# Optimization experiments

Hardware: AMD Instinct MI355X
Metric: run time of the kernel (lower is better)

## Reference

```python
import jax, jax.numpy as jnp
import numpy as np

S = 8192        # seq_length
H2 = 1024       # 2 * lstm_hidden_size
A = 2048        # attention_hidden_size
E = 768         # embedding_dim == pos_embedding_dim


def _bahdanau_weights(sentence, length, ctx, W_s, b_s, W_c, b_c, v, b_v):
    # sentence: [1, S, H2], ctx: [1, E_ctx]
    u = jnp.einsum('bsh,ha->bsa', sentence, W_s) + b_s \
        + (ctx @ W_c + b_c)[:, None, :]                    # [1, S, A]
    e = jnp.einsum('bsa,a->bs', jnp.tanh(u), v) + b_v       # [1, S]
    mask = jnp.arange(S)[None, :] >= length[:, None]        # [1, S] key mask
    e = jnp.where(mask, -jnp.inf, e)
    all_inf = jnp.all(mask, axis=1)                         # [1]
    # guard fully-masked rows so softmax stays finite, then zero them (matches torch)
    e_safe = jnp.where(all_inf[:, None], jnp.zeros_like(e), e)
    w = jax.nn.softmax(e_safe, axis=1)
    return jnp.where(all_inf[:, None], 0.0, w)              # [1, S]


def setup_inputs() -> dict:
    key = jax.random.key(0)
    ks = jax.random.split(key, 24)
    f = jax.random.normal
    sc_s = 1.0 / np.sqrt(H2)
    sc_c = 1.0 / np.sqrt(E)
    sc_v = 1.0 / np.sqrt(A)
    inp = {
        'sentence': f(ks[0], (1, S, H2), jnp.float32),
        'length': jax.random.randint(ks[1], (1,), 0, S),
        'pos_embedding': f(ks[2], (1, E), jnp.float32),
        'cardinal_phrase_embedding': f(ks[3], (1, E), jnp.float32),
        'headline_embedding': f(ks[4], (1, E), jnp.float32),
    }
    i = 5
    for tag in ('p', 'c', 'h'):
        inp[f'W_sent_{tag}'] = f(ks[i], (H2, A), jnp.float32) * sc_s; i += 1
        inp[f'b_sent_{tag}'] = f(ks[i], (A,), jnp.float32) * sc_s; i += 1
        inp[f'W_ctx_{tag}'] = f(ks[i], (E, A), jnp.float32) * sc_c; i += 1
        inp[f'b_ctx_{tag}'] = f(ks[i], (A,), jnp.float32) * sc_c; i += 1
        inp[f'v_{tag}'] = f(ks[i], (A,), jnp.float32) * sc_v; i += 1
        inp[f'bv_{tag}'] = f(ks[i], (), jnp.float32) * sc_v; i += 1
    return inp


def reference(sentence, length, pos_embedding, cardinal_phrase_embedding,
              headline_embedding,
              W_sent_p, b_sent_p, W_ctx_p, b_ctx_p, v_p, bv_p,
              W_sent_c, b_sent_c, W_ctx_c, b_ctx_c, v_c, bv_c,
              W_sent_h, b_sent_h, W_ctx_h, b_ctx_h, v_h, bv_h):
    w_pos = _bahdanau_weights(sentence, length, pos_embedding,
                              W_sent_p, b_sent_p, W_ctx_p, b_ctx_p, v_p, bv_p)
    w_card = _bahdanau_weights(sentence, length, cardinal_phrase_embedding,
                               W_sent_c, b_sent_c, W_ctx_c, b_ctx_c, v_c, bv_c)
    w_head = _bahdanau_weights(sentence, length, headline_embedding,
                               W_sent_h, b_sent_h, W_ctx_h, b_ctx_h, v_h, bv_h)
    fused = (w_pos + w_card + w_head) / 3.0                 # [1, S]
    return jnp.einsum('bs,bsh->bh', fused, sentence)        # [1, H2]
```

## Files before the change

kernel.cpp:

```cpp
#include <hip/hip_runtime.h>
#include <hip/hip_bf16.h>
#include <stdint.h>


namespace {

constexpr int S = 8192;
constexpr int H = 1024;
constexpr int A = 2048;
constexpr int E = 768;

typedef __bf16 bf16x8 __attribute__((ext_vector_type(8)));
typedef float f32x4 __attribute__((ext_vector_type(4)));

__device__ __forceinline__ void gl_lds16(const void* g, void* l) {
  __builtin_amdgcn_global_load_lds(
      (const __attribute__((address_space(1))) void*)g,
      (__attribute__((address_space(3))) void*)l, 16, 0, 0);
}

__global__ __launch_bounds__(256)
void k_prep(const float* __restrict__ sentence, __bf16* __restrict__ sentB,
            const float* __restrict__ Wp, const float* __restrict__ Wc_s,
            const float* __restrict__ Wh, __bf16* __restrict__ WtB,
            const float* __restrict__ ctx_p, const float* __restrict__ ctx_c,
            const float* __restrict__ ctx_h,
            const float* __restrict__ Wcx_p, const float* __restrict__ Wcx_c,
            const float* __restrict__ Wcx_h,
            const float* __restrict__ bs_p, const float* __restrict__ bs_c,
            const float* __restrict__ bs_h,
            const float* __restrict__ bc_p, const float* __restrict__ bc_c,
            const float* __restrict__ bc_h,
            float* __restrict__ ctxb, float* __restrict__ e_arr,
            float* __restrict__ outz, const int* __restrict__ length) {
  __shared__ float tile[64][65];
  __shared__ float part[4][64];
  int b = blockIdx.x;
  int t = threadIdx.x;

  if (b < 4096) {
    int len = min(max(length[0], 0), S);
    if (b * 2 >= len) return;
    int g = b * 256 + t;
    const float4* s4 = (const float4*)sentence + (size_t)g * 2;
    float4 a = s4[0], c = s4[1];
    bf16x8 o;
    o[0] = (__bf16)a.x; o[1] = (__bf16)a.y; o[2] = (__bf16)a.z; o[3] = (__bf16)a.w;
    o[4] = (__bf16)c.x; o[5] = (__bf16)c.y; o[6] = (__bf16)c.z; o[7] = (__bf16)c.w;
    *((bf16x8*)sentB + g) = o;
  } else if (b < 5632) {
    int r = b - 4096;
    int head = r >> 9; r &= 511;
    const float* W = head == 0 ? Wp : (head == 1 ? Wc_s : Wh);
    __bf16* dst = WtB + (size_t)head * A * H;
    int a0 = (r & 31) * 64;
    int k0 = (r >> 5) * 64;
#pragma unroll
    for (int i = 0; i < 16; ++i) {
      int idx = t + i * 256;
      int rr = idx >> 6, cc = idx & 63;
      tile[cc][rr] = W[(size_t)(k0 + rr) * A + a0 + cc];
    }
    __syncthreads();
    int al = t >> 3, kg = (t & 7) * 8;
#pragma unroll
    for (int half = 0; half < 2; ++half) {
      int aa = al + half * 32;
      bf16x8 o;
#pragma unroll
      for (int j = 0; j < 8; ++j) o[j] = (__bf16)tile[aa][kg + j];
      *(bf16x8*)&dst[(size_t)(a0 + aa) * H + k0 + kg] = o;
    }
  } else if (b < 5728) {
    int r = b - 5632;
    int head = r >> 5; r &= 31;
    const float* ctx = head == 0 ? ctx_p : (head == 1 ? ctx_c : ctx_h);
    const float* Wc  = head == 0 ? Wcx_p : (head == 1 ? Wcx_c : Wcx_h);
    int a0 = r * 64;
    int al = t & 63, slice = t >> 6;
    int a = a0 + al;
    float s = 0.f;
    int e0 = slice * 192;
#pragma unroll 8
    for (int e = e0; e < e0 + 192; ++e) s = fmaf(ctx[e], Wc[(size_t)e * A + a], s);
    part[slice][al] = s;
    __syncthreads();
    if (t < 64) {
      const float* bs = head == 0 ? bs_p : (head == 1 ? bs_c : bs_h);
      const float* bc = head == 0 ? bc_p : (head == 1 ? bc_c : bc_h);
      ctxb[head * A + a0 + t] = part[0][t] + part[1][t] + part[2][t] + part[3][t]
                              + bs[a0 + t] + bc[a0 + t];
    }
  } else if (b < 5752) {
    int g = (b - 5728) * 256 + t;
    ((float4*)e_arr)[g] = (float4){0.f, 0.f, 0.f, 0.f};
  } else {
    ((float4*)outz)[t] = (float4){0.f, 0.f, 0.f, 0.f};
  }
}

__global__ __launch_bounds__(256)
void k_gemm_e(const __bf16* __restrict__ sentB, const __bf16* __restrict__ WtB,
              const float* __restrict__ ctxb,
              const float* __restrict__ v_p, const float* __restrict__ v_c,
              const float* __restrict__ v_h,
              const int* __restrict__ length, float* __restrict__ e_out) {
  int m0 = blockIdx.x * 128;
  int len = length[0];
  if (m0 >= len) return;
  int n0 = blockIdx.y * 128;
  int head = blockIdx.z;
  const float* v  = head == 0 ? v_p : (head == 1 ? v_c : v_h);
  const __bf16* Wt = WtB + (size_t)head * A * H;
  const float* cb = ctxb + head * A;
  float* e_h = e_out + head * S;

  __shared__ __align__(16) __bf16 lsA[128 * 32];
  __shared__ __align__(16) __bf16 lsB[128 * 32];
  __shared__ float e_part[128];

  int tid = threadIdx.x;
  if (tid < 128) e_part[tid] = 0.f;

  int lane = tid & 63;
  int wave = tid >> 6;
  int wm = wave >> 1, wn = wave & 1;
  int quad = lane >> 4, l16 = lane & 15;

  f32x4 acc[4][4];
#pragma unroll
  for (int i = 0; i < 4; ++i)
#pragma unroll
    for (int j = 0; j < 4; ++j) acc[i][j] = (f32x4){0.f, 0.f, 0.f, 0.f};

  const __bf16* gA0 = sentB + (size_t)(m0 + (tid >> 2)) * H + ((tid & 3) * 8);
  const __bf16* gA1 = gA0 + (size_t)64 * H;
  const __bf16* gB0 = Wt + (size_t)(n0 + (tid >> 2)) * H + ((tid & 3) * 8);
  const __bf16* gB1 = gB0 + (size_t)64 * H;

  for (int k0 = 0; k0 < H; k0 += 32) {
    __syncthreads();
    gl_lds16(gA0 + k0, lsA + tid * 8);
    gl_lds16(gA1 + k0, lsA + 2048 + tid * 8);
    gl_lds16(gB0 + k0, lsB + tid * 8);
    gl_lds16(gB1 + k0, lsB + 2048 + tid * 8);
    __syncthreads();

    bf16x8 af[4], bfv[4];
#pragma unroll
    for (int i = 0; i < 4; ++i) {
      af[i]  = *(const bf16x8*)&lsA[(wm * 64 + i * 16 + l16) * 32 + quad * 8];
      bfv[i] = *(const bf16x8*)&lsB[(wn * 64 + i * 16 + l16) * 32 + quad * 8];
    }
#pragma unroll
    for (int i = 0; i < 4; ++i)
#pragma unroll
      for (int j = 0; j < 4; ++j)
        acc[i][j] = __builtin_amdgcn_mfma_f32_16x16x32_bf16(af[i], bfv[j], acc[i][j], 0, 0, 0);
  }

  float vj[4], cbj[4];
#pragma unroll
  for (int j = 0; j < 4; ++j) {
    int col = n0 + wn * 64 + j * 16 + l16;
    vj[j] = v[col];
    cbj[j] = cb[col];
  }
#pragma unroll
  for (int i = 0; i < 4; ++i) {
#pragma unroll
    for (int r = 0; r < 4; ++r) {
      float p = 0.f;
#pragma unroll
      for (int j = 0; j < 4; ++j) {
        float u = acc[i][j][r] + cbj[j];
        float ex = __expf(2.f * u);
        float th = 1.f - 2.f / (ex + 1.f);
        p = fmaf(th, vj[j], p);
      }
      p += __shfl_xor(p, 1);
      p += __shfl_xor(p, 2);
      p += __shfl_xor(p, 4);
      p += __shfl_xor(p, 8);
      if (l16 == 0) atomicAdd(&e_part[wm * 64 + i * 16 + quad * 4 + r], p);
    }
  }
  __syncthreads();
  if (tid < 128) atomicAdd(&e_h[m0 + tid], e_part[tid]);
}

__global__ __launch_bounds__(1024)
void k_sum(const float* __restrict__ e_arr, const int* __restrict__ length,
           float* __restrict__ sums) {
  int head = blockIdx.x;
  const float* e_h = e_arr + head * S;
  int len = min(max(length[0], 0), S);
  int t = threadIdx.x;
  __shared__ float red[16];

  float ss = 0.f;
  int base = t * 8;
#pragma unroll
  for (int j = 0; j < 8; ++j) {
    int s = base + j;
    if (s < len) ss += __expf(e_h[s]);
  }
#pragma unroll
  for (int o = 32; o >= 1; o >>= 1) ss += __shfl_xor(ss, o);
  if ((t & 63) == 0) red[t >> 6] = ss;
  __syncthreads();
  if (t == 0) {
    float tot = 0.f;
#pragma unroll
    for (int i = 0; i < 16; ++i) tot += red[i];
    sums[head] = tot;
  }
}

__global__ void k_out(const float* __restrict__ sent, const float* __restrict__ e_arr,
                      const float* __restrict__ sums, const int* __restrict__ length,
                      float* __restrict__ out) {
  int len = min(max(length[0], 0), S);
  int r0 = blockIdx.x * 32;
  if (r0 >= len) return;
  int col = threadIdx.x * 4;
  int rend = min(r0 + 32, len);
  float i0 = 1.f / sums[0], i1 = 1.f / sums[1], i2 = 1.f / sums[2];
  float4 acc = {0.f, 0.f, 0.f, 0.f};
  for (int r = r0; r < rend; ++r) {
    float w = (__expf(e_arr[r]) * i0 +
               __expf(e_arr[S + r]) * i1 +
               __expf(e_arr[2 * S + r]) * i2) * (1.f / 3.f);
    float4 x = *(const float4*)(sent + (size_t)r * H + col);
    acc.x = fmaf(w, x.x, acc.x);
    acc.y = fmaf(w, x.y, acc.y);
    acc.z = fmaf(w, x.z, acc.z);
    acc.w = fmaf(w, x.w, acc.w);
  }
  atomicAdd(&out[col + 0], acc.x);
  atomicAdd(&out[col + 1], acc.y);
  atomicAdd(&out[col + 2], acc.z);
  atomicAdd(&out[col + 3], acc.w);
}

}

extern "C" void kernel_launch(void* const* d_in, const int* in_sizes, int n_in,
                              void* d_out, int out_size, void* d_ws, size_t ws_size,
                              hipStream_t stream) {
  const float* sentence = (const float*)d_in[0];
  const int* length     = (const int*)d_in[1];
  const float* ctx_p = (const float*)d_in[2];
  const float* ctx_c = (const float*)d_in[3];
  const float* ctx_h = (const float*)d_in[4];
  const float* W_s[3] = {(const float*)d_in[5],  (const float*)d_in[11], (const float*)d_in[17]};
  const float* b_s[3] = {(const float*)d_in[6],  (const float*)d_in[12], (const float*)d_in[18]};
  const float* W_c[3] = {(const float*)d_in[7],  (const float*)d_in[13], (const float*)d_in[19]};
  const float* b_c[3] = {(const float*)d_in[8],  (const float*)d_in[14], (const float*)d_in[20]};
  const float* v_[3]  = {(const float*)d_in[9],  (const float*)d_in[15], (const float*)d_in[21]};
  float* out = (float*)d_out;

  char* ws = (char*)d_ws;
  __bf16* sentB = (__bf16*)(ws);
  __bf16* WtB   = (__bf16*)(ws + 16777216);
  float* ctxb   = (float*)(ws + 29360128);
  float* e_arr  = (float*)(ws + 29384704);
  float* sums   = (float*)(ws + 29483008);

  k_prep<<<5753, 256, 0, stream>>>(sentence, sentB,
                                   W_s[0], W_s[1], W_s[2], WtB,
                                   ctx_p, ctx_c, ctx_h,
                                   W_c[0], W_c[1], W_c[2],
                                   b_s[0], b_s[1], b_s[2],
                                   b_c[0], b_c[1], b_c[2],
                                   ctxb, e_arr, out, length);
  k_gemm_e<<<dim3(S / 128, A / 128, 3), 256, 0, stream>>>(sentB, WtB, ctxb,
                                                          v_[0], v_[1], v_[2], length, e_arr);
  k_sum<<<3, 1024, 0, stream>>>(e_arr, length, sums);
  k_out<<<S / 32, 256, 0, stream>>>(sentence, e_arr, sums, length, out);
}
```

Measured before the change: 234.6 us.

## Fuse all stages into one persistent cooperative kernel with grid syncs

Replaces the four separate launches (prep, GEMM+tanh reduction, softmax sum, weighted output) with a single cooperative kernel of 512 persistent blocks that loop over the former block indices and separate phases with grid.sync. The softmax denominators are now computed redundantly in every block instead of in a separate kernel, removing the sums buffer. This aims to remove inter-kernel launch gaps, at the cost of lower parallelism per phase, grid-wide barrier overhead, and repeated reads of the score array by every block.

```diff
diff --git a/kernel.cpp b/kernel.cpp
--- a/kernel.cpp
+++ b/kernel.cpp
@@ -1,7 +1,10 @@
 #include <hip/hip_runtime.h>
 #include <hip/hip_bf16.h>
+#include <hip/hip_cooperative_groups.h>
 #include <stdint.h>
 
+
+namespace cg = cooperative_groups;
 
 namespace {
 
@@ -9,9 +12,26 @@
 constexpr int H = 1024;
 constexpr int A = 2048;
 constexpr int E = 768;
+constexpr int GRID = 512;
 
 typedef __bf16 bf16x8 __attribute__((ext_vector_type(8)));
 typedef float f32x4 __attribute__((ext_vector_type(4)));
+
+struct KArgs {
+  const float* sentence;
+  const int* length;
+  const float* ctx[3];
+  const float* Ws[3];
+  const float* bs[3];
+  const float* Wc[3];
+  const float* bc[3];
+  const float* v[3];
+  __bf16* sentB;
+  __bf16* WtB;
+  float* ctxb;
+  float* e_arr;
+  float* out;
+};
 
 __device__ __forceinline__ void gl_lds16(const void* g, void* l) {
   __builtin_amdgcn_global_load_lds(
@@ -19,228 +39,206 @@
       (__attribute__((address_space(3))) void*)l, 16, 0, 0);
 }
 
-__global__ __launch_bounds__(256)
-void k_prep(const float* __restrict__ sentence, __bf16* __restrict__ sentB,
-            const float* __restrict__ Wp, const float* __restrict__ Wc_s,
-            const float* __restrict__ Wh, __bf16* __restrict__ WtB,
-            const float* __restrict__ ctx_p, const float* __restrict__ ctx_c,
-            const float* __restrict__ ctx_h,
-            const float* __restrict__ Wcx_p, const float* __restrict__ Wcx_c,
-            const float* __restrict__ Wcx_h,
-            const float* __restrict__ bs_p, const float* __restrict__ bs_c,
-            const float* __restrict__ bs_h,
-            const float* __restrict__ bc_p, const float* __restrict__ bc_c,
-            const float* __restrict__ bc_h,
-            float* __restrict__ ctxb, float* __restrict__ e_arr,
-            float* __restrict__ outz, const int* __restrict__ length) {
-  __shared__ float tile[64][65];
-  __shared__ float part[4][64];
-  int b = blockIdx.x;
-  int t = threadIdx.x;
-
-  if (b < 4096) {
-    int len = min(max(length[0], 0), S);
-    if (b * 2 >= len) return;
-    int g = b * 256 + t;
-    const float4* s4 = (const float4*)sentence + (size_t)g * 2;
-    float4 a = s4[0], c = s4[1];
-    bf16x8 o;
-    o[0] = (__bf16)a.x; o[1] = (__bf16)a.y; o[2] = (__bf16)a.z; o[3] = (__bf16)a.w;
-    o[4] = (__bf16)c.x; o[5] = (__bf16)c.y; o[6] = (__bf16)c.z; o[7] = (__bf16)c.w;
-    *((bf16x8*)sentB + g) = o;
-  } else if (b < 5632) {
-    int r = b - 4096;
-    int head = r >> 9; r &= 511;
-    const float* W = head == 0 ? Wp : (head == 1 ? Wc_s : Wh);
-    __bf16* dst = WtB + (size_t)head * A * H;
-    int a0 = (r & 31) * 64;
-    int k0 = (r >> 5) * 64;
-#pragma unroll
-    for (int i = 0; i < 16; ++i) {
-      int idx = t + i * 256;
-      int rr = idx >> 6, cc = idx & 63;
-      tile[cc][rr] = W[(size_t)(k0 + rr) * A + a0 + cc];
+__global__ __launch_bounds__(256, 2)
+void k_mega(KArgs a) {
+  __shared__ __align__(16) union {
+    struct { float tile[64][65]; float part[4][64]; } p;
+    struct { __bf16 lsA[4096]; __bf16 lsB[4096]; float e_part[128]; } g;
+    struct { float red[3][4]; } o;
+  } sh;
+
+  cg::grid_group grid = cg::this_grid();
+  const int bid = blockIdx.x;
+  const int t = threadIdx.x;
+  const int len = min(max(a.length[0], 0), S);
+
+  for (int it = bid; it < 5753; it += GRID) {
+    if (it < 4096) {
+      if (it * 2 >= len) continue;
+      int g = it * 256 + t;
+      const float4* s4 = (const float4*)a.sentence + (size_t)g * 2;
+      float4 x = s4[0], y = s4[1];
+      bf16x8 o;
+      o[0] = (__bf16)x.x; o[1] = (__bf16)x.y; o[2] = (__bf16)x.z; o[3] = (__bf16)x.w;
+      o[4] = (__bf16)y.x; o[5] = (__bf16)y.y; o[6] = (__bf16)y.z; o[7] = (__bf16)y.w;
+      *((bf16x8*)a.sentB + g) = o;
+    } else if (it < 5632) {
+      int r = it - 4096;
+      int head = r >> 9; r &= 511;
+      const float* W = a.Ws[head];
+      __bf16* dst = a.WtB + (size_t)head * A * H;
+      int a0 = (r & 31) * 64;
+      int k0 = (r >> 5) * 64;
+      __syncthreads();
+#pragma unroll
+      for (int i = 0; i < 16; ++i) {
+        int idx = t + i * 256;
+        int rr = idx >> 6, cc = idx & 63;
+        sh.p.tile[cc][rr] = W[(size_t)(k0 + rr) * A + a0 + cc];
+      }
+      __syncthreads();
+      int al = t >> 3, kg = (t & 7) * 8;
+#pragma unroll
+      for (int half = 0; half < 2; ++half) {
+        int aa = al + half * 32;
+        bf16x8 o;
+#pragma unroll
+        for (int j = 0; j < 8; ++j) o[j] = (__bf16)sh.p.tile[aa][kg + j];
+        *(bf16x8*)&dst[(size_t)(a0 + aa) * H + k0 + kg] = o;
+      }
+    } else if (it < 5728) {
+      int r = it - 5632;
+      int head = r >> 5; r &= 31;
+      const float* cx = a.ctx[head];
+      const float* Wc = a.Wc[head];
+      int a0 = r * 64;
+      int al = t & 63, slice = t >> 6;
+      float s = 0.f;
+      int e0 = slice * 192;
+#pragma unroll 8
+      for (int e = e0; e < e0 + 192; ++e) s = fmaf(cx[e], Wc[(size_t)e * A + a0 + al], s);
+      __syncthreads();
+      sh.p.part[slice][al] = s;
+      __syncthreads();
+      if (t < 64) {
+        a.ctxb[head * A + a0 + t] = sh.p.part[0][t] + sh.p.part[1][t] + sh.p.part[2][t] +
+                                    sh.p.part[3][t] + a.bs[head][a0 + t] + a.bc[head][a0 + t];
+      }
+    } else if (it < 5752) {
+      int g = (it - 5728) * 256 + t;
+      ((float4*)a.e_arr)[g] = (float4){0.f, 0.f, 0.f, 0.f};
+    } else {
+      ((float4*)a.out)[t] = (float4){0.f, 0.f, 0.f, 0.f};
+    }
+  }
+
+  grid.sync();
+
+  for (int j = bid; j < 3072; j += GRID) {
+    int head = j >> 10;
+    int r = j & 1023;
+    int m0 = (r & 63) << 7;
+    int n0 = (r >> 6) << 7;
+    if (m0 >= len) continue;
+
+    const float* v = a.v[head];
+    const __bf16* Wt = a.WtB + (size_t)head * A * H;
+    const float* cb = a.ctxb + head * A;
+    float* e_h = a.e_arr + head * S;
+
+    int lane = t & 63;
+    int wave = t >> 6;
+    int wm = wave >> 1, wn = wave & 1;
+    int quad = lane >> 4, l16 = lane & 15;
+
+    if (t < 128) sh.g.e_part[t] = 0.f;
+
+    f32x4 acc[4][4];
+#pragma unroll
+    for (int i = 0; i < 4; ++i)
+#pragma unroll
+      for (int jj = 0; jj < 4; ++jj) acc[i][jj] = (f32x4){0.f, 0.f, 0.f, 0.f};
+
+    const __bf16* gA0 = a.sentB + (size_t)(m0 + (t >> 2)) * H + ((t & 3) * 8);
+    const __bf16* gA1 = gA0 + (size_t)64 * H;
+    const __bf16* gB0 = Wt + (size_t)(n0 + (t >> 2)) * H + ((t & 3) * 8);
+    const __bf16* gB1 = gB0 + (size_t)64 * H;
+
+    for (int k0 = 0; k0 < H; k0 += 32) {
+      __syncthreads();
+      gl_lds16(gA0 + k0, sh.g.lsA + t * 8);
+      gl_lds16(gA1 + k0, sh.g.lsA + 2048 + t * 8);
+      gl_lds16(gB0 + k0, sh.g.lsB + t * 8);
+      gl_lds16(gB1 + k0, sh.g.lsB + 2048 + t * 8);
+      __syncthreads();
+
+      bf16x8 af[4], bfv[4];
+#pragma unroll
+      for (int i = 0; i < 4; ++i) {
+        af[i]  = *(const bf16x8*)&sh.g.lsA[(wm * 64 + i * 16 + l16) * 32 + quad * 8];
+        bfv[i] = *(const bf16x8*)&sh.g.lsB[(wn * 64 + i * 16 + l16) * 32 + quad * 8];
+      }
+#pragma unroll
+      for (int i = 0; i < 4; ++i)
+#pragma unroll
+        for (int jj = 0; jj < 4; ++jj)
+          acc[i][jj] = __builtin_amdgcn_mfma_f32_16x16x32_bf16(af[i], bfv[jj], acc[i][jj], 0, 0, 0);
+    }
+
+    float vj[4], cbj[4];
+#pragma unroll
+    for (int jj = 0; jj < 4; ++jj) {
+      int col = n0 + wn * 64 + jj * 16 + l16;
+      vj[jj] = v[col];
+      cbj[jj] = cb[col];
+    }
+#pragma unroll
+    for (int i = 0; i < 4; ++i) {
+#pragma unroll
+      for (int rr = 0; rr < 4; ++rr) {
+        float p = 0.f;
+#pragma unroll
+        for (int jj = 0; jj < 4; ++jj) {
+          float u = acc[i][jj][rr] + cbj[jj];
+          float ex = __expf(2.f * u);
+          float th = 1.f - 2.f / (ex + 1.f);
+          p = fmaf(th, vj[jj], p);
+        }
+        p += __shfl_xor(p, 1);
+        p += __shfl_xor(p, 2);
+        p += __shfl_xor(p, 4);
+        p += __shfl_xor(p, 8);
+        if (l16 == 0) atomicAdd(&sh.g.e_part[wm * 64 + i * 16 + quad * 4 + rr], p);
+      }
     }
     __syncthreads();
-    int al = t >> 3, kg = (t & 7) * 8;
-#pragma unroll
-    for (int half = 0; half < 2; ++half) {
-      int aa = al + half * 32;
-      bf16x8 o;
-#pragma unroll
-      for (int j = 0; j < 8; ++j) o[j] = (__bf16)tile[aa][kg + j];
-      *(bf16x8*)&dst[(size_t)(a0 + aa) * H + k0 + kg] = o;
-    }
-  } else if (b < 5728) {
-    int r = b - 5632;
-    int head = r >> 5; r &= 31;
-    const float* ctx = head == 0 ? ctx_p : (head == 1 ? ctx_c : ctx_h);
-    const float* Wc  = head == 0 ? Wcx_p : (head == 1 ? Wcx_c : Wcx_h);
-    int a0 = r * 64;
-    int al = t & 63, slice = t >> 6;
-    int a = a0 + al;
-    float s = 0.f;
-    int e0 = slice * 192;
-#pragma unroll 8
-    for (int e = e0; e < e0 + 192; ++e) s = fmaf(ctx[e], Wc[(size_t)e * A + a], s);
-    part[slice][al] = s;
-    __syncthreads();
-    if (t < 64) {
-      const float* bs = head == 0 ? bs_p : (head == 1 ? bs_c : bs_h);
-      const float* bc = head == 0 ? bc_p : (head == 1 ? bc_c : bc_h);
-      ctxb[head * A + a0 + t] = part[0][t] + part[1][t] + part[2][t] + part[3][t]
-                              + bs[a0 + t] + bc[a0 + t];
-    }
-  } else if (b < 5752) {
-    int g = (b - 5728) * 256 + t;
-    ((float4*)e_arr)[g] = (float4){0.f, 0.f, 0.f, 0.f};
-  } else {
-    ((float4*)outz)[t] = (float4){0.f, 0.f, 0.f, 0.f};
-  }
-}
-
-__global__ __launch_bounds__(256)
-void k_gemm_e(const __bf16* __restrict__ sentB, const __bf16* __restrict__ WtB,
-              const float* __restrict__ ctxb,
-              const float* __restrict__ v_p, const float* __restrict__ v_c,
-              const float* __restrict__ v_h,
-              const int* __restrict__ length, float* __restrict__ e_out) {
-  int m0 = blockIdx.x * 128;
-  int len = length[0];
-  if (m0 >= len) return;
-  int n0 = blockIdx.y * 128;
-  int head = blockIdx.z;
-  const float* v  = head == 0 ? v_p : (head == 1 ? v_c : v_h);
-  const __bf16* Wt = WtB + (size_t)head * A * H;
-  const float* cb = ctxb + head * A;
-  float* e_h = e_out + head * S;
-
-  __shared__ __align__(16) __bf16 lsA[128 * 32];
-  __shared__ __align__(16) __bf16 lsB[128 * 32];
-  __shared__ float e_part[128];
-
-  int tid = threadIdx.x;
-  if (tid < 128) e_part[tid] = 0.f;
-
-  int lane = tid & 63;
-  int wave = tid >> 6;
-  int wm = wave >> 1, wn = wave & 1;
-  int quad = lane >> 4, l16 = lane & 15;
-
-  f32x4 acc[4][4];
-#pragma unroll
-  for (int i = 0; i < 4; ++i)
-#pragma unroll
-    for (int j = 0; j < 4; ++j) acc[i][j] = (f32x4){0.f, 0.f, 0.f, 0.f};
-
-  const __bf16* gA0 = sentB + (size_t)(m0 + (tid >> 2)) * H + ((tid & 3) * 8);
-  const __bf16* gA1 = gA0 + (size_t)64 * H;
-  const __bf16* gB0 = Wt + (size_t)(n0 + (tid >> 2)) * H + ((tid & 3) * 8);
-  const __bf16* gB1 = gB0 + (size_t)64 * H;
-
-  for (int k0 = 0; k0 < H; k0 += 32) {
-    __syncthreads();
-    gl_lds16(gA0 + k0, lsA + tid * 8);
-    gl_lds16(gA1 + k0, lsA + 2048 + tid * 8);
-    gl_lds16(gB0 + k0, lsB + tid * 8);
-    gl_lds16(gB1 + k0, lsB + 2048 + tid * 8);
-    __syncthreads();
-
-    bf16x8 af[4], bfv[4];
-#pragma unroll
-    for (int i = 0; i < 4; ++i) {
-      af[i]  = *(const bf16x8*)&lsA[(wm * 64 + i * 16 + l16) * 32 + quad * 8];
-      bfv[i] = *(const bf16x8*)&lsB[(wn * 64 + i * 16 + l16) * 32 + quad * 8];
-    }
-#pragma unroll
-    for (int i = 0; i < 4; ++i)
-#pragma unroll
-      for (int j = 0; j < 4; ++j)
-        acc[i][j] = __builtin_amdgcn_mfma_f32_16x16x32_bf16(af[i], bfv[j], acc[i][j], 0, 0, 0);
-  }
-
-  float vj[4], cbj[4];
-#pragma unroll
-  for (int j = 0; j < 4; ++j) {
-    int col = n0 + wn * 64 + j * 16 + l16;
-    vj[j] = v[col];
-    cbj[j] = cb[col];
-  }
-#pragma unroll
-  for (int i = 0; i < 4; ++i) {
-#pragma unroll
-    for (int r = 0; r < 4; ++r) {
-      float p = 0.f;
-#pragma unroll
-      for (int j = 0; j < 4; ++j) {
-        float u = acc[i][j][r] + cbj[j];
-        float ex = __expf(2.f * u);
-        float th = 1.f - 2.f / (ex + 1.f);
-        p = fmaf(th, vj[j], p);
-      }
-      p += __shfl_xor(p, 1);
-      p += __shfl_xor(p, 2);
-      p += __shfl_xor(p, 4);
-      p += __shfl_xor(p, 8);
-      if (l16 == 0) atomicAdd(&e_part[wm * 64 + i * 16 + quad * 4 + r], p);
-    }
+    if (t < 128) atomicAdd(&e_h[m0 + t], sh.g.e_part[t]);
+  }
+
+  grid.sync();
+
+  float t0 = 0.f, t1 = 0.f, t2 = 0.f;
+  for (int s = t; s < len; s += 256) {
+    t0 += __expf(a.e_arr[s]);
+    t1 += __expf(a.e_arr[S + s]);
+    t2 += __expf(a.e_arr[2 * S + s]);
+  }
+#pragma unroll
+  for (int o = 32; o >= 1; o >>= 1) {
+    t0 += __shfl_xor(t0, o);
+    t1 += __shfl_xor(t1, o);
+    t2 += __shfl_xor(t2, o);
+  }
+  if ((t & 63) == 0) {
+    int w = t >> 6;
+    sh.o.red[0][w] = t0; sh.o.red[1][w] = t1; sh.o.red[2][w] = t2;
   }
   __syncthreads();
-  if (tid < 128) atomicAdd(&e_h[m0 + tid], e_part[tid]);
-}
-
-__global__ __launch_bounds__(1024)
-void k_sum(const float* __restrict__ e_arr, const int* __restrict__ length,
-           float* __restrict__ sums) {
-  int head = blockIdx.x;
-  const float* e_h = e_arr + head * S;
-  int len = min(max(length[0], 0), S);
-  int t = threadIdx.x;
-  __shared__ float red[16];
-
-  float ss = 0.f;
-  int base = t * 8;
-#pragma unroll
-  for (int j = 0; j < 8; ++j) {
-    int s = base + j;
-    if (s < len) ss += __expf(e_h[s]);
-  }
-#pragma unroll
-  for (int o = 32; o >= 1; o >>= 1) ss += __shfl_xor(ss, o);
-  if ((t & 63) == 0) red[t >> 6] = ss;
-  __syncthreads();
-  if (t == 0) {
-    float tot = 0.f;
-#pragma unroll
-    for (int i = 0; i < 16; ++i) tot += red[i];
-    sums[head] = tot;
-  }
-}
-
-__global__ void k_out(const float* __restrict__ sent, const float* __restrict__ e_arr,
-                      const float* __restrict__ sums, const int* __restrict__ length,
-                      float* __restrict__ out) {
-  int len = min(max(length[0], 0), S);
-  int r0 = blockIdx.x * 32;
-  if (r0 >= len) return;
-  int col = threadIdx.x * 4;
-  int rend = min(r0 + 32, len);
-  float i0 = 1.f / sums[0], i1 = 1.f / sums[1], i2 = 1.f / sums[2];
-  float4 acc = {0.f, 0.f, 0.f, 0.f};
-  for (int r = r0; r < rend; ++r) {
-    float w = (__expf(e_arr[r]) * i0 +
-               __expf(e_arr[S + r]) * i1 +
-               __expf(e_arr[2 * S + r]) * i2) * (1.f / 3.f);
-    float4 x = *(const float4*)(sent + (size_t)r * H + col);
-    acc.x = fmaf(w, x.x, acc.x);
-    acc.y = fmaf(w, x.y, acc.y);
-    acc.z = fmaf(w, x.z, acc.z);
-    acc.w = fmaf(w, x.w, acc.w);
-  }
-  atomicAdd(&out[col + 0], acc.x);
-  atomicAdd(&out[col + 1], acc.y);
-  atomicAdd(&out[col + 2], acc.z);
-  atomicAdd(&out[col + 3], acc.w);
+  float i0 = 1.f / (sh.o.red[0][0] + sh.o.red[0][1] + sh.o.red[0][2] + sh.o.red[0][3]);
+  float i1 = 1.f / (sh.o.red[1][0] + sh.o.red[1][1] + sh.o.red[1][2] + sh.o.red[1][3]);
+  float i2 = 1.f / (sh.o.red[2][0] + sh.o.red[2][1] + sh.o.red[2][2] + sh.o.red[2][3]);
+
+  for (int it = bid; it < 256; it += GRID) {
+    int r0 = it * 32;
+    if (r0 >= len) continue;
+    int col = t * 4;
+    int rend = min(r0 + 32, len);
+    float4 acc4 = {0.f, 0.f, 0.f, 0.f};
+    for (int rr = r0; rr < rend; ++rr) {
+      float w = (__expf(a.e_arr[rr]) * i0 +
+                 __expf(a.e_arr[S + rr]) * i1 +
+                 __expf(a.e_arr[2 * S + rr]) * i2) * (1.f / 3.f);
+      float4 x = *(const float4*)(a.sentence + (size_t)rr * H + col);
+      acc4.x = fmaf(w, x.x, acc4.x);
+      acc4.y = fmaf(w, x.y, acc4.y);
+      acc4.z = fmaf(w, x.z, acc4.z);
+      acc4.w = fmaf(w, x.w, acc4.w);
+    }
+    atomicAdd(&a.out[col + 0], acc4.x);
+    atomicAdd(&a.out[col + 1], acc4.y);
+    atomicAdd(&a.out[col + 2], acc4.z);
+    atomicAdd(&a.out[col + 3], acc4.w);
+  }
 }
 
 }
@@ -248,34 +246,27 @@
 extern "C" void kernel_launch(void* const* d_in, const int* in_sizes, int n_in,
                               void* d_out, int out_size, void* d_ws, size_t ws_size,
                               hipStream_t stream) {
-  const float* sentence = (const float*)d_in[0];
-  const int* length     = (const int*)d_in[1];
-  const float* ctx_p = (const float*)d_in[2];
-  const float* ctx_c = (const float*)d_in[3];
-  const float* ctx_h = (const float*)d_in[4];
-  const float* W_s[3] = {(const float*)d_in[5],  (const float*)d_in[11], (const float*)d_in[17]};
-  const float* b_s[3] = {(const float*)d_in[6],  (const float*)d_in[12], (const float*)d_in[18]};
-  const float* W_c[3] = {(const float*)d_in[7],  (const float*)d_in[13], (const float*)d_in[19]};
-  const float* b_c[3] = {(const float*)d_in[8],  (const float*)d_in[14], (const float*)d_in[20]};
-  const float* v_[3]  = {(const float*)d_in[9],  (const float*)d_in[15], (const float*)d_in[21]};
-  float* out = (float*)d_out;
-
   char* ws = (char*)d_ws;
-  __bf16* sentB = (__bf16*)(ws);
-  __bf16* WtB   = (__bf16*)(ws + 16777216);
-  float* ctxb   = (float*)(ws + 29360128);
-  float* e_arr  = (float*)(ws + 29384704);
-  float* sums   = (float*)(ws + 29483008);
-
-  k_prep<<<5753, 256, 0, stream>>>(sentence, sentB,
-                                   W_s[0], W_s[1], W_s[2], WtB,
-                                   ctx_p, ctx_c, ctx_h,
-                                   W_c[0], W_c[1], W_c[2],
-                                   b_s[0], b_s[1], b_s[2],
-                                   b_c[0], b_c[1], b_c[2],
-                                   ctxb, e_arr, out, length);
-  k_gemm_e<<<dim3(S / 128, A / 128, 3), 256, 0, stream>>>(sentB, WtB, ctxb,
-                                                          v_[0], v_[1], v_[2], length, e_arr);
-  k_sum<<<3, 1024, 0, stream>>>(e_arr, length, sums);
-  k_out<<<S / 32, 256, 0, stream>>>(sentence, e_arr, sums, length, out);
-}
+  KArgs ka;
+  ka.sentence = (const float*)d_in[0];
+  ka.length   = (const int*)d_in[1];
+  ka.ctx[0] = (const float*)d_in[2];
+  ka.ctx[1] = (const float*)d_in[3];
+  ka.ctx[2] = (const float*)d_in[4];
+  for (int h = 0; h < 3; ++h) {
+    int base = 5 + h * 6;
+    ka.Ws[h] = (const float*)d_in[base + 0];
+    ka.bs[h] = (const float*)d_in[base + 1];
+    ka.Wc[h] = (const float*)d_in[base + 2];
+    ka.bc[h] = (const float*)d_in[base + 3];
+    ka.v[h]  = (const float*)d_in[base + 4];
+  }
+  ka.sentB = (__bf16*)(ws);
+  ka.WtB   = (__bf16*)(ws + 16777216);
+  ka.ctxb  = (float*)(ws + 29360128);
+  ka.e_arr = (float*)(ws + 29384704);
+  ka.out   = (float*)d_out;
+
+  void* params[] = { (void*)&ka };
+  hipLaunchCooperativeKernel((const void*)k_mega, dim3(GRID), dim3(256), params, 0, stream);
+}
```

New measurement: 463.4 us. 97.6% more time.
